# Performance work log

Hardware: AMD Instinct MI355X
Metric: run time of the kernel (lower is better)

Reference implementation:

```python
import jax, jax.numpy as jnp
import numpy as np

B, L, H, N = 8, 2048, 512, 64  # batch, seq_len, d_model, SSM state size


def setup_inputs() -> dict:
    key = jax.random.key(0)
    ks = jax.random.split(key, 10)
    x = jax.random.normal(ks[0], (B, L, H), jnp.float32)
    # S4D-style parameters (diagonal SSM, S4D-Lin init)
    log_dt = jnp.log(1e-3) + jax.random.uniform(ks[1], (H,), jnp.float32) * (jnp.log(1e-1) - jnp.log(1e-3))
    A_re = -0.5 * jnp.ones((H, N), jnp.float32)
    A_im = jnp.tile(np.pi * jnp.arange(N, dtype=np.float32), (H, 1))
    C_re = jax.random.normal(ks[2], (H, N), jnp.float32) * (0.5 ** 0.5)
    C_im = jax.random.normal(ks[3], (H, N), jnp.float32) * (0.5 ** 0.5)
    D_skip = jax.random.normal(ks[4], (H,), jnp.float32)
    # S4 output linear (GLU): d_model -> 2*d_model, then gated
    W_out = jax.random.normal(ks[5], (2 * H, H), jnp.float32) / np.sqrt(H)
    b_out = jnp.zeros((2 * H,), jnp.float32)
    # LayerNorms
    g1 = jnp.ones((H,), jnp.float32); beta1 = jnp.zeros((H,), jnp.float32)
    g2 = jnp.ones((H,), jnp.float32); beta2 = jnp.zeros((H,), jnp.float32)
    # 1x1 conv FFN (kernel_size=1 => pointwise linear), d_ff = d_model
    W1 = jax.random.normal(ks[6], (H, H), jnp.float32) / np.sqrt(H)
    bc1 = jnp.zeros((H,), jnp.float32)
    W2 = jax.random.normal(ks[7], (H, H), jnp.float32) / np.sqrt(H)
    bc2 = jnp.zeros((H,), jnp.float32)
    return dict(x=x, log_dt=log_dt, A_re=A_re, A_im=A_im, C_re=C_re, C_im=C_im,
                D_skip=D_skip, W_out=W_out, b_out=b_out, g1=g1, beta1=beta1,
                g2=g2, beta2=beta2, W1=W1, bc1=bc1, W2=W2, bc2=bc2)


def _layer_norm(x, g, b):
    mu = jnp.mean(x, axis=-1, keepdims=True)
    var = jnp.mean((x - mu) ** 2, axis=-1, keepdims=True)
    return (x - mu) / jnp.sqrt(var + 1e-5) * g + b


def _s4(x, log_dt, A_re, A_im, C_re, C_im, D_skip, W_out, b_out):
    # x: (B, L, H) channels-last (transposed=False)
    Lx = x.shape[1]
    dt = jnp.exp(log_dt)                       # (H,)
    A = A_re + 1j * A_im                       # (H, N) diagonal state matrix
    dtA = A * dt[:, None]
    # ZOH discretization of C: Ct = C * (exp(dt*A) - 1) / A
    Ct = (C_re + 1j * C_im) * ((jnp.exp(dtA) - 1.0) / A)
    # Vandermonde kernel: K[h, l] = 2 Re sum_n Ct[h,n] exp(dt*A[h,n]*l)
    l = jnp.arange(Lx, dtype=jnp.float32)
    K = 2.0 * jnp.real(jnp.einsum('hn,hnl->hl', Ct, jnp.exp(dtA[:, :, None] * l)))
    # FFT long convolution (linear conv via zero-padded circular conv)
    u = jnp.swapaxes(x, 1, 2)                  # (B, H, L)
    n = 2 * Lx
    y = jnp.fft.irfft(jnp.fft.rfft(u, n) * jnp.fft.rfft(K, n)[None], n)[..., :Lx]
    y = y + D_skip[None, :, None] * u          # skip connection D*u
    y = jax.nn.gelu(y)                         # S4 default activation
    # output linear + GLU (S4 default postact)
    z = jnp.einsum('bhl,fh->bfl', y, W_out) + b_out[None, :, None]
    a, g = jnp.split(z, 2, axis=1)
    y = a * jax.nn.sigmoid(g)
    return jnp.swapaxes(y, 1, 2)               # (B, L, H)


def reference(x, log_dt, A_re, A_im, C_re, C_im, D_skip, W_out, b_out,
              g1, beta1, g2, beta2, W1, bc1, W2, bc2):
    new_x = _s4(x, log_dt, A_re, A_im, C_re, C_im, D_skip, W_out, b_out)
    x = x + new_x
    x = _layer_norm(x, g1, beta1)
    # FFN via 1x1 convs (pointwise linears); dropout is identity in eval
    y = jax.nn.relu(jnp.einsum('blh,fh->blf', x, W1) + bc1)
    y = jnp.einsum('blf,hf->blh', y, W2) + bc2
    return _layer_norm(x + y, g2, beta2)
```

## Files before the change

### kernel.cpp

```cpp
#include <hip/hip_runtime.h>
#include <cstddef>
#include <cstdint>

#define B_DIM 8
#define L_DIM 2048
#define H_DIM 512
#define N_DIM 64
#define HN (H_DIM * N_DIM)
#define BLH (B_DIM * L_DIM * H_DIM)
#define M_DIM (B_DIM * L_DIM)

typedef unsigned short u16;
typedef short bf16x8 __attribute__((ext_vector_type(8)));
typedef float floatx4 __attribute__((ext_vector_type(4)));

__device__ __forceinline__ float sigmoidf_(float v) {
    return 1.0f / (1.0f + __expf(-v));
}

__device__ __forceinline__ float gelu_tanh_(float x) {
    float x3 = x * x * x;
    float z = 0.7978845608028654f * fmaf(0.044715f, x3, x);
    float e = __expf(-2.0f * fabsf(z));
    float th = (1.0f - e) / (1.0f + e);
    th = copysignf(th, z);
    return 0.5f * x * (1.0f + th);
}

__device__ __forceinline__ u16 f2b(float f) {
    unsigned u = __float_as_uint(f);
    unsigned r = (u + 0x7fffu + ((u >> 16) & 1u)) >> 16;
    return (u16)r;
}
__device__ __forceinline__ float b2f(u16 u) {
    return __uint_as_float(((unsigned)u) << 16);
}
__device__ __forceinline__ void unpack2(unsigned u, float& a, float& b) {
    a = __uint_as_float(u << 16);
    b = __uint_as_float(u & 0xffff0000u);
}
__device__ __forceinline__ unsigned pack2(float a, float b) {
    return (unsigned)f2b(a) | ((unsigned)f2b(b) << 16);
}

__device__ __forceinline__ void csq(float& r, float& i) {
    float nr = r * r - i * i;
    i = 2.0f * r * i;
    r = nr;
}

__global__ __launch_bounds__(256) void cast_kernel(
    const float* __restrict__ src, u16* __restrict__ dst)
{
    int i = blockIdx.x * 256 + threadIdx.x;
    float4 v = *(const float4*)(src + (size_t)i * 4);
    uint2 p;
    p.x = pack2(v.x, v.y);
    p.y = pack2(v.z, v.w);
    *(uint2*)(dst + (size_t)i * 4) = p;
}

__global__ __launch_bounds__(256) void precompute_kernel(
    const float* __restrict__ log_dt, const float* __restrict__ A_re,
    const float* __restrict__ A_im, const float* __restrict__ C_re,
    const float* __restrict__ C_im, float* __restrict__ P)
{
    int i = blockIdx.x * 256 + threadIdx.x;
    if (i >= HN) return;
    int h = i >> 6;
    float dt = expf(log_dt[h]);
    float Ar = A_re[i], Ai = A_im[i];
    float ar = dt * Ar, ai = dt * Ai;
    float e = expf(ar);
    float wr = e * cosf(ai);
    float wi = e * sinf(ai);
    float em1r = wr - 1.0f, em1i = wi;
    float inv = 1.0f / fmaf(Ar, Ar, Ai * Ai);
    float qr = fmaf(em1r, Ar, em1i * Ai) * inv;
    float qi = fmaf(em1i, Ar, -(em1r * Ai)) * inv;
    float Cr = C_re[i], Ci = C_im[i];
    float ctr = Cr * qr - Ci * qi;
    float cti = Cr * qi + Ci * qr;
    P[i]          = wr;
    P[HN + i]     = wi;
    P[2 * HN + i] = 2.0f * ctr;
    P[3 * HN + i] = 2.0f * cti;
}

__global__ __launch_bounds__(256) void ktab_kernel(
    const float* __restrict__ P, float* __restrict__ Ktab)
{
    int wv = threadIdx.x >> 6, lane = threadIdx.x & 63;
    int h = blockIdx.x * 4 + wv;
    int pidx = (h << 6) + lane;
    float wr = P[pidx], wi = P[HN + pidx];
    float c2r = P[2 * HN + pidx], c2i = P[3 * HN + pidx];
    float pr = 1.0f, pi = 0.0f;
    for (int tau = 0; tau < 64; ++tau) {
        float term = c2r * pr - c2i * pi;
        #pragma unroll
        for (int m = 32; m > 0; m >>= 1) term += __shfl_xor(term, m, 64);
        if (lane == 0) Ktab[(h << 6) + tau] = term;
        float nr = pr * wr - pi * wi, ni = pr * wi + pi * wr;
        pr = nr; pi = ni;
    }
}

__global__ __launch_bounds__(256) void toepfill_kernel(
    const float* __restrict__ Ktab, u16* __restrict__ Toep_bf)
{
    int idx = blockIdx.x * 256 + threadIdx.x;
    int h = idx >> 12;
    int rem = idx & 4095;
    int tt = rem >> 6, j = rem & 63;
    u16 v = 0;
    if (j <= tt) v = f2b(Ktab[(h << 6) + (tt - j)]);
    Toep_bf[idx] = v;
}

__global__ __launch_bounds__(256) void xtrans_kernel(
    const float* __restrict__ x, u16* __restrict__ XT)
{
    __shared__ float tile[32][33];
    int b  = blockIdx.z;
    int l0 = blockIdx.x * 32;
    int h0 = blockIdx.y * 32;
    int tx = threadIdx.x & 31;
    int ty = threadIdx.x >> 5;
    #pragma unroll
    for (int r = 0; r < 4; ++r)
        tile[ty + r * 8][tx] = x[((size_t)b * L_DIM + l0 + ty + r * 8) * H_DIM + h0 + tx];
    __syncthreads();
    #pragma unroll
    for (int r = 0; r < 4; ++r)
        XT[((size_t)b * H_DIM + h0 + ty + r * 8) * L_DIM + l0 + tx] = f2b(tile[tx][ty + r * 8]);
}

__global__ __launch_bounds__(256) void ssm_chunk_kernel(
    const u16* __restrict__ XT, const float* __restrict__ P,
    const u16* __restrict__ Toep_bf, const float* __restrict__ D_skip,
    u16* __restrict__ YT)
{
    __shared__ u16 U[128 * 72];
    __shared__ u16 S[128 * 136];
    __shared__ u16 EVT[13312];
    u16* E  = EVT;
    u16* Tp = EVT;
    u16* V  = EVT + 4608;

    const int h    = blockIdx.x;
    const int b0   = blockIdx.y * 4;
    const int t    = threadIdx.x;
    const int lane = t & 63;
    const int wv   = t >> 6;
    const int lm   = lane & 15, lq = lane >> 4;

    const int pidx = (h << 6) + lane;
    const float wr  = P[pidx],          wi  = P[HN + pidx];
    const float c2r = P[2 * HN + pidx], c2i = P[3 * HN + pidx];

    #pragma unroll
    for (int r = 0; r < 4; ++r) {
        int idx = t + r * 256;
        int row = idx >> 3, ch = idx & 7;
        const u16* gp = XT + (((size_t)(b0 + (row >> 5)) * H_DIM + h) << 11)
                           + ((row & 31) << 6) + (ch << 3);
        *(uint4*)&U[row * 72 + ch * 8] = *(const uint4*)gp;
    }

    float bwr, bwi;
    {
        float g16r = wr, g16i = wi;
        csq(g16r, g16i); csq(g16r, g16i); csq(g16r, g16i); csq(g16r, g16i);
        if (wv == 0)      { bwr = 1.0f; bwi = 0.0f; }
        else if (wv == 1) { bwr = g16r; bwi = g16i; }
        else if (wv == 2) { bwr = g16r; bwi = g16i; csq(bwr, bwi); }
        else {
            float g32r = g16r, g32i = g16i; csq(g32r, g32i);
            bwr = g32r * g16r - g32i * g16i;
            bwi = g32r * g16i + g32i * g16r;
        }
    }

    {
        float pr = bwr, pi = bwi;
        #pragma unroll
        for (int jk = 0; jk < 16; ++jk) {
            int k = (wv << 4) + jk;
            int j = 63 - k;
            E[(2 * lane) * 72 + j]     = f2b(pr);
            E[(2 * lane + 1) * 72 + j] = f2b(pi);
            float nr = pr * wr - pi * wi, ni = pr * wi + pi * wr;
            pr = nr; pi = ni;
        }
    }
    __syncthreads();

    {
        const int wm = wv >> 1, wn = wv & 1;
        floatx4 acc[4][4] = {};
        #pragma unroll
        for (int ks = 0; ks < 2; ++ks) {
            bf16x8 af[4], bfv[4];
            #pragma unroll
            for (int i = 0; i < 4; ++i)
                af[i] = *(const bf16x8*)&E[(wm * 64 + i * 16 + lm) * 72 + ks * 32 + lq * 8];
            #pragma unroll
            for (int j = 0; j < 4; ++j)
                bfv[j] = *(const bf16x8*)&U[(wn * 64 + j * 16 + lm) * 72 + ks * 32 + lq * 8];
            #pragma unroll
            for (int i = 0; i < 4; ++i) {
                #pragma unroll
                for (int j = 0; j < 4; ++j)
                    acc[i][j] = __builtin_amdgcn_mfma_f32_16x16x32_bf16(af[i], bfv[j], acc[i][j], 0, 0, 0);
            }
        }
        #pragma unroll
        for (int i = 0; i < 4; ++i) {
            #pragma unroll
            for (int j = 0; j < 4; ++j) {
                int ncol = wn * 64 + j * 16 + lm;
                int m0   = wm * 64 + i * 16 + lq * 4;
                u16 pk[4];
                #pragma unroll
                for (int r = 0; r < 4; ++r) pk[r] = f2b(acc[i][j][r]);
                *(uint2*)&S[ncol * 136 + m0] = *(uint2*)pk;
            }
        }
    }
    __syncthreads();

    {
        float pr = bwr, pi = bwi;
        {
            float nr = pr * wr - pi * wi, ni = pr * wi + pi * wr;
            pr = nr; pi = ni;
        }
        #pragma unroll
        for (int jk = 1; jk <= 16; ++jk) {
            int tr = (wv << 4) + jk - 1;
            float qr = c2r * pr - c2i * pi;
            float qi = c2r * pi + c2i * pr;
            V[tr * 136 + 2 * lane]     = f2b(qr);
            V[tr * 136 + 2 * lane + 1] = f2b(-qi);
            float nr = pr * wr - pi * wi, ni = pr * wi + pi * wr;
            pr = nr; pi = ni;
        }
        #pragma unroll
        for (int r = 0; r < 2; ++r) {
            int idx = t + r * 256;
            int row = idx >> 3, ch = idx & 7;
            *(uint4*)&Tp[row * 72 + ch * 8] =
                *(const uint4*)&Toep_bf[((size_t)h << 12) + (row << 6) + (ch << 3)];
        }
        float wTr = wr, wTi = wi;
        csq(wTr, wTi); csq(wTr, wTi); csq(wTr, wTi);
        csq(wTr, wTi); csq(wTr, wTi); csq(wTr, wTi);
        float Sr = 0.0f, Si = 0.0f;
        const int n2 = lane * 2;
        for (int c = 0; c < 32; ++c) {
            int base = (wv * 32 + c) * 136 + n2;
            unsigned lv = *(unsigned*)&S[base];
            float lr, li;
            unpack2(lv, lr, li);
            *(unsigned*)&S[base] = pack2(Sr, Si);
            float nSr = wTr * Sr - wTi * Si + lr;
            Si = wTr * Si + wTi * Sr + li;
            Sr = nSr;
        }
    }
    __syncthreads();

    {
        const float Dh = D_skip[h];
        floatx4 acc[4][2] = {};
        #pragma unroll
        for (int ks = 0; ks < 6; ++ks) {
            bf16x8 af[4], bfv[2];
            if (ks < 2) {
                #pragma unroll
                for (int i = 0; i < 4; ++i)
                    af[i] = *(const bf16x8*)&Tp[(i * 16 + lm) * 72 + ks * 32 + lq * 8];
                #pragma unroll
                for (int j = 0; j < 2; ++j)
                    bfv[j] = *(const bf16x8*)&U[(wv * 32 + j * 16 + lm) * 72 + ks * 32 + lq * 8];
            } else {
                #pragma unroll
                for (int i = 0; i < 4; ++i)
                    af[i] = *(const bf16x8*)&V[(i * 16 + lm) * 136 + (ks - 2) * 32 + lq * 8];
                #pragma unroll
                for (int j = 0; j < 2; ++j)
                    bfv[j] = *(const bf16x8*)&S[(wv * 32 + j * 16 + lm) * 136 + (ks - 2) * 32 + lq * 8];
            }
            #pragma unroll
            for (int i = 0; i < 4; ++i) {
                #pragma unroll
                for (int j = 0; j < 2; ++j)
                    acc[i][j] = __builtin_amdgcn_mfma_f32_16x16x32_bf16(af[i], bfv[j], acc[i][j], 0, 0, 0);
            }
        }
        #pragma unroll
        for (int j = 0; j < 2; ++j) {
            int ncol = wv * 32 + j * 16 + lm;
            int bloc = ncol >> 5, c = ncol & 31;
            size_t gbase = (((size_t)(b0 + bloc) * H_DIM + h) << 11) + (c << 6);
            #pragma unroll
            for (int i = 0; i < 4; ++i) {
                int t0 = i * 16 + lq * 4;
                u16 upk[4];
                *(uint2*)upk = *(const uint2*)&U[ncol * 72 + t0];
                u16 opk[4];
                #pragma unroll
                for (int r = 0; r < 4; ++r) {
                    float uvv = b2f(upk[r]);
                    float yv = gelu_tanh_(fmaf(Dh, uvv, acc[i][j][r]));
                    opk[r] = f2b(yv);
                }
                *(uint2*)&YT[gbase + t0] = *(uint2*)opk;
            }
        }
    }
}

__global__ __launch_bounds__(256) void ytrans_kernel(
    const u16* __restrict__ YT, u16* __restrict__ Y)
{
    __shared__ u16 tile[32][33];
    int b  = blockIdx.z;
    int l0 = blockIdx.x * 32;
    int h0 = blockIdx.y * 32;
    int tx = threadIdx.x & 31;
    int ty = threadIdx.x >> 5;
    #pragma unroll
    for (int r = 0; r < 4; ++r)
        tile[ty + r * 8][tx] = YT[((size_t)b * H_DIM + h0 + ty + r * 8) * L_DIM + l0 + tx];
    __syncthreads();
    #pragma unroll
    for (int r = 0; r < 4; ++r)
        Y[((size_t)b * L_DIM + l0 + ty + r * 8) * H_DIM + h0 + tx] = tile[tx][ty + r * 8];
}

__device__ __forceinline__ void stage_tile_512(
    const u16* __restrict__ g, u16* lds, int row0, int k0)
{
    const int t = threadIdx.x;
    const int row  = t >> 2;
    const int csrc = (t & 3) ^ ((t >> 3) & 3);
    const u16* gp = g + (size_t)(row0 + row) * 512 + k0 + csrc * 8;
    __builtin_amdgcn_global_load_lds(
        (const __attribute__((address_space(1))) unsigned int*)gp,
        (__attribute__((address_space(3))) unsigned int*)(lds + (size_t)t * 8),
        16, 0, 0);
}

__global__ __launch_bounds__(512) void gemm1_glu_kernel(
    const u16* __restrict__ A, const u16* __restrict__ Wo,
    const float* __restrict__ bo, const float* __restrict__ x,
    u16* __restrict__ out)
{
    __shared__ u16 As[2][128 * 32];
    __shared__ u16 Ba[2][128 * 32];
    __shared__ u16 Bg[2][128 * 32];
    const int t    = threadIdx.x;
    const int lane = t & 63;
    const int wv   = t >> 6;
    const int wm   = wv >> 2, wn = wv & 3;
    const int lm   = lane & 15, lq = lane >> 4;
    const int sw   = (lq ^ ((lm >> 1) & 3)) * 8;
    const int m0   = blockIdx.x * 128, n0 = blockIdx.y * 128;
    floatx4 accA[4][2] = {};
    floatx4 accG[4][2] = {};

    stage_tile_512(A, As[0], m0, 0);
    stage_tile_512(Wo, Ba[0], n0, 0);
    stage_tile_512(Wo, Bg[0], 512 + n0, 0);
    __syncthreads();

    int cur = 0;
    for (int k0 = 32; k0 < 512; k0 += 32) {
        const int nx = cur ^ 1;
        stage_tile_512(A, As[nx], m0, k0);
        stage_tile_512(Wo, Ba[nx], n0, k0);
        stage_tile_512(Wo, Bg[nx], 512 + n0, k0);

        bf16x8 af[4], ba[2], bg[2];
        #pragma unroll
        for (int i = 0; i < 4; ++i)
            af[i] = *(const bf16x8*)&As[cur][(wm * 64 + i * 16 + lm) * 32 + sw];
        #pragma unroll
        for (int j = 0; j < 2; ++j) {
            ba[j] = *(const bf16x8*)&Ba[cur][(wn * 32 + j * 16 + lm) * 32 + sw];
            bg[j] = *(const bf16x8*)&Bg[cur][(wn * 32 + j * 16 + lm) * 32 + sw];
        }
        #pragma unroll
        for (int i = 0; i < 4; ++i) {
            #pragma unroll
            for (int j = 0; j < 2; ++j) {
                accA[i][j] = __builtin_amdgcn_mfma_f32_16x16x32_bf16(af[i], ba[j], accA[i][j], 0, 0, 0);
                accG[i][j] = __builtin_amdgcn_mfma_f32_16x16x32_bf16(af[i], bg[j], accG[i][j], 0, 0, 0);
            }
        }
        __syncthreads();
        cur = nx;
    }
    {
        bf16x8 af[4], ba[2], bg[2];
        #pragma unroll
        for (int i = 0; i < 4; ++i)
            af[i] = *(const bf16x8*)&As[cur][(wm * 64 + i * 16 + lm) * 32 + sw];
        #pragma unroll
        for (int j = 0; j < 2; ++j) {
            ba[j] = *(const bf16x8*)&Ba[cur][(wn * 32 + j * 16 + lm) * 32 + sw];
            bg[j] = *(const bf16x8*)&Bg[cur][(wn * 32 + j * 16 + lm) * 32 + sw];
        }
        #pragma unroll
        for (int i = 0; i < 4; ++i) {
            #pragma unroll
            for (int j = 0; j < 2; ++j) {
                accA[i][j] = __builtin_amdgcn_mfma_f32_16x16x32_bf16(af[i], ba[j], accA[i][j], 0, 0, 0);
                accG[i][j] = __builtin_amdgcn_mfma_f32_16x16x32_bf16(af[i], bg[j], accG[i][j], 0, 0, 0);
            }
        }
    }
    #pragma unroll
    for (int j = 0; j < 2; ++j) {
        int n = n0 + wn * 32 + j * 16 + lm;
        float bav = bo[n], bgv = bo[512 + n];
        #pragma unroll
        for (int i = 0; i < 4; ++i) {
            #pragma unroll
            for (int r = 0; r < 4; ++r) {
                int m = m0 + wm * 64 + i * 16 + lq * 4 + r;
                float av = accA[i][j][r] + bav;
                float gv = accG[i][j][r] + bgv;
                float xv = x[(size_t)m * 512 + n];
                out[(size_t)m * 512 + n] = f2b(fmaf(av, sigmoidf_(gv), xv));
            }
        }
    }
}

template<int EPI>
__global__ __launch_bounds__(512) void gemm_bt_bf_kernel(
    const u16* __restrict__ A, const u16* __restrict__ Bw,
    const float* __restrict__ bias, u16* __restrict__ C)
{
    __shared__ u16 As[2][128 * 32];
    __shared__ u16 Bs[2][128 * 32];
    const int t    = threadIdx.x;
    const int lane = t & 63;
    const int wv   = t >> 6;
    const int wm   = wv >> 2, wn = wv & 3;
    const int lm   = lane & 15, lq = lane >> 4;
    const int sw   = (lq ^ ((lm >> 1) & 3)) * 8;
    const int m0   = blockIdx.x * 128, n0 = blockIdx.y * 128;
    floatx4 acc[4][2] = {};

    stage_tile_512(A, As[0], m0, 0);
    stage_tile_512(Bw, Bs[0], n0, 0);
    __syncthreads();

    int cur = 0;
    for (int k0 = 32; k0 < 512; k0 += 32) {
        const int nx = cur ^ 1;
        stage_tile_512(A, As[nx], m0, k0);
        stage_tile_512(Bw, Bs[nx], n0, k0);

        bf16x8 af[4], bfr[2];
        #pragma unroll
        for (int i = 0; i < 4; ++i)
            af[i] = *(const bf16x8*)&As[cur][(wm * 64 + i * 16 + lm) * 32 + sw];
        #pragma unroll
        for (int j = 0; j < 2; ++j)
            bfr[j] = *(const bf16x8*)&Bs[cur][(wn * 32 + j * 16 + lm) * 32 + sw];
        #pragma unroll
        for (int i = 0; i < 4; ++i) {
            #pragma unroll
            for (int j = 0; j < 2; ++j)
                acc[i][j] = __builtin_amdgcn_mfma_f32_16x16x32_bf16(af[i], bfr[j], acc[i][j], 0, 0, 0);
        }
        __syncthreads();
        cur = nx;
    }
    {
        bf16x8 af[4], bfr[2];
        #pragma unroll
        for (int i = 0; i < 4; ++i)
            af[i] = *(const bf16x8*)&As[cur][(wm * 64 + i * 16 + lm) * 32 + sw];
        #pragma unroll
        for (int j = 0; j < 2; ++j)
            bfr[j] = *(const bf16x8*)&Bs[cur][(wn * 32 + j * 16 + lm) * 32 + sw];
        #pragma unroll
        for (int i = 0; i < 4; ++i) {
            #pragma unroll
            for (int j = 0; j < 2; ++j)
                acc[i][j] = __builtin_amdgcn_mfma_f32_16x16x32_bf16(af[i], bfr[j], acc[i][j], 0, 0, 0);
        }
    }
    #pragma unroll
    for (int j = 0; j < 2; ++j) {
        int n = n0 + wn * 32 + j * 16 + lm;
        float bv = bias[n];
        #pragma unroll
        for (int i = 0; i < 4; ++i) {
            #pragma unroll
            for (int r = 0; r < 4; ++r) {
                int m = m0 + wm * 64 + i * 16 + lq * 4 + r;
                float v = acc[i][j][r] + bv;
                if (EPI == 1) v = fmaxf(v, 0.0f);
                C[(size_t)m * 512 + n] = f2b(v);
            }
        }
    }
}

template<bool HASRES, bool F32OUT>
__global__ __launch_bounds__(256) void ln_bf_kernel(
    const u16* __restrict__ in, const u16* __restrict__ res,
    const float* __restrict__ gamma, const float* __restrict__ beta,
    u16* __restrict__ outb, float* __restrict__ outf)
{
    int w    = threadIdx.x >> 6;
    int lane = threadIdx.x & 63;
    size_t row  = (size_t)blockIdx.x * 4 + w;
    size_t base = row * 512 + lane * 8;
    uint4 raw = *(const uint4*)(in + base);
    float v[8];
    unpack2(raw.x, v[0], v[1]); unpack2(raw.y, v[2], v[3]);
    unpack2(raw.z, v[4], v[5]); unpack2(raw.w, v[6], v[7]);
    if (HASRES) {
        uint4 rr = *(const uint4*)(res + base);
        float rv[8];
        unpack2(rr.x, rv[0], rv[1]); unpack2(rr.y, rv[2], rv[3]);
        unpack2(rr.z, rv[4], rv[5]); unpack2(rr.w, rv[6], rv[7]);
        #pragma unroll
        for (int i = 0; i < 8; ++i) v[i] += rv[i];
    }
    float s = 0.0f, sq = 0.0f;
    #pragma unroll
    for (int i = 0; i < 8; ++i) { s += v[i]; sq = fmaf(v[i], v[i], sq); }
    #pragma unroll
    for (int m = 32; m > 0; m >>= 1) {
        s  += __shfl_xor(s, m, 64);
        sq += __shfl_xor(sq, m, 64);
    }
    float mu  = s * (1.0f / 512.0f);
    float var = sq * (1.0f / 512.0f) - mu * mu;
    float rs  = rsqrtf(var + 1e-5f);
    float g[8], bt[8];
    *(float4*)&g[0]  = *(const float4*)(gamma + lane * 8);
    *(float4*)&g[4]  = *(const float4*)(gamma + lane * 8 + 4);
    *(float4*)&bt[0] = *(const float4*)(beta + lane * 8);
    *(float4*)&bt[4] = *(const float4*)(beta + lane * 8 + 4);
    float o[8];
    #pragma unroll
    for (int i = 0; i < 8; ++i)
        o[i] = fmaf((v[i] - mu) * rs, g[i], bt[i]);
    if (F32OUT) {
        *(float4*)(outf + base)     = *(float4*)&o[0];
        *(float4*)(outf + base + 4) = *(float4*)&o[4];
    } else {
        uint4 p;
        p.x = pack2(o[0], o[1]); p.y = pack2(o[2], o[3]);
        p.z = pack2(o[4], o[5]); p.w = pack2(o[6], o[7]);
        *(uint4*)(outb + base) = p;
    }
}

extern "C" void kernel_launch(void* const* d_in, const int* in_sizes, int n_in,
                              void* d_out, int out_size, void* d_ws, size_t ws_size,
                              hipStream_t stream)
{
    (void)in_sizes; (void)n_in; (void)out_size; (void)ws_size;
    const float* x      = (const float*)d_in[0];
    const float* log_dt = (const float*)d_in[1];
    const float* A_re   = (const float*)d_in[2];
    const float* A_im   = (const float*)d_in[3];
    const float* C_re   = (const float*)d_in[4];
    const float* C_im   = (const float*)d_in[5];
    const float* D_skip = (const float*)d_in[6];
    const float* W_out  = (const float*)d_in[7];
    const float* b_out  = (const float*)d_in[8];
    const float* g1     = (const float*)d_in[9];
    const float* beta1  = (const float*)d_in[10];
    const float* g2     = (const float*)d_in[11];
    const float* beta2  = (const float*)d_in[12];
    const float* W1     = (const float*)d_in[13];
    const float* bc1    = (const float*)d_in[14];
    const float* W2     = (const float*)d_in[15];
    const float* bc2    = (const float*)d_in[16];
    float* out = (float*)d_out;

    char*  wsb    = (char*)d_ws;
    float* P      = (float*)wsb;
    float* Ktab   = (float*)(wsb + 4 * HN * 4);
    u16*   Toep   = (u16*)(wsb + 4 * HN * 4 + 512 * 64 * 4);
    u16*   Wobf   = Toep + 512 * 4096;
    u16*   W1bf   = Wobf + 1024 * 512;
    u16*   W2bf   = W1bf + 512 * 512;
    u16*   r1     = W2bf + 512 * 512;
    u16*   r2     = r1 + BLH;
    u16*   r3     = r2 + BLH;

    cast_kernel<<<512, 256, 0, stream>>>(W_out, Wobf);
    cast_kernel<<<256, 256, 0, stream>>>(W1, W1bf);
    cast_kernel<<<256, 256, 0, stream>>>(W2, W2bf);
    precompute_kernel<<<HN / 256, 256, 0, stream>>>(log_dt, A_re, A_im, C_re, C_im, P);
    ktab_kernel<<<128, 256, 0, stream>>>(P, Ktab);
    toepfill_kernel<<<8192, 256, 0, stream>>>(Ktab, Toep);
    xtrans_kernel<<<dim3(L_DIM / 32, H_DIM / 32, B_DIM), 256, 0, stream>>>(x, r1);
    ssm_chunk_kernel<<<dim3(H_DIM, 2), 256, 0, stream>>>(r1, P, Toep, D_skip, r2);
    ytrans_kernel<<<dim3(L_DIM / 32, H_DIM / 32, B_DIM), 256, 0, stream>>>(r2, r3);
    gemm1_glu_kernel<<<dim3(M_DIM / 128, 4), 512, 0, stream>>>(r3, Wobf, b_out, x, r2);
    ln_bf_kernel<false, false><<<M_DIM / 4, 256, 0, stream>>>(r2, nullptr, g1, beta1, r1, nullptr);
    gemm_bt_bf_kernel<1><<<dim3(M_DIM / 128, 4), 512, 0, stream>>>(r1, W1bf, bc1, r3);
    gemm_bt_bf_kernel<0><<<dim3(M_DIM / 128, 4), 512, 0, stream>>>(r3, W2bf, bc2, r2);
    ln_bf_kernel<true, true><<<M_DIM / 4, 256, 0, stream>>>(r2, r1, g2, beta2, nullptr, out);
}
```

Baseline: 250.6 us.

## Fuse second FFN GEMM with residual LayerNorm and merge small setup kernels

```diff
diff --git a/kernel.cpp b/kernel.cpp
--- a/kernel.cpp
+++ b/kernel.cpp
@@ -49,10 +49,17 @@
     r = nr;
 }
 
-__global__ __launch_bounds__(256) void cast_kernel(
-    const float* __restrict__ src, u16* __restrict__ dst)
-{
-    int i = blockIdx.x * 256 + threadIdx.x;
+__global__ __launch_bounds__(256) void cast3_kernel(
+    const float* __restrict__ s0, const float* __restrict__ s1,
+    const float* __restrict__ s2, u16* __restrict__ d0,
+    u16* __restrict__ d1, u16* __restrict__ d2)
+{
+    int bid = blockIdx.x;
+    const float* src; u16* dst; int off;
+    if (bid < 512)      { src = s0; dst = d0; off = bid; }
+    else if (bid < 768) { src = s1; dst = d1; off = bid - 512; }
+    else                { src = s2; dst = d2; off = bid - 768; }
+    int i = off * 256 + threadIdx.x;
     float4 v = *(const float4*)(src + (size_t)i * 4);
     uint2 p;
     p.x = pack2(v.x, v.y);
@@ -60,14 +67,18 @@
     *(uint2*)(dst + (size_t)i * 4) = p;
 }
 
-__global__ __launch_bounds__(256) void precompute_kernel(
+__global__ __launch_bounds__(256) void params_kernel(
     const float* __restrict__ log_dt, const float* __restrict__ A_re,
     const float* __restrict__ A_im, const float* __restrict__ C_re,
-    const float* __restrict__ C_im, float* __restrict__ P)
-{
-    int i = blockIdx.x * 256 + threadIdx.x;
-    if (i >= HN) return;
-    int h = i >> 6;
+    const float* __restrict__ C_im, float* __restrict__ P,
+    u16* __restrict__ Toep_bf)
+{
+    __shared__ float ktab_s[4][64];
+    const int t = threadIdx.x;
+    const int wv = t >> 6, lane = t & 63;
+    const int i = blockIdx.x * 256 + t;
+    const int h = i >> 6;
+
     float dt = expf(log_dt[h]);
     float Ar = A_re[i], Ai = A_im[i];
     float ar = dt * Ar, ai = dt * Ai;
@@ -79,43 +90,38 @@
     float qr = fmaf(em1r, Ar, em1i * Ai) * inv;
     float qi = fmaf(em1i, Ar, -(em1r * Ai)) * inv;
     float Cr = C_re[i], Ci = C_im[i];
-    float ctr = Cr * qr - Ci * qi;
-    float cti = Cr * qi + Ci * qr;
+    float c2r = 2.0f * (Cr * qr - Ci * qi);
+    float c2i = 2.0f * (Cr * qi + Ci * qr);
     P[i]          = wr;
     P[HN + i]     = wi;
-    P[2 * HN + i] = 2.0f * ctr;
-    P[3 * HN + i] = 2.0f * cti;
-}
-
-__global__ __launch_bounds__(256) void ktab_kernel(
-    const float* __restrict__ P, float* __restrict__ Ktab)
-{
-    int wv = threadIdx.x >> 6, lane = threadIdx.x & 63;
-    int h = blockIdx.x * 4 + wv;
-    int pidx = (h << 6) + lane;
-    float wr = P[pidx], wi = P[HN + pidx];
-    float c2r = P[2 * HN + pidx], c2i = P[3 * HN + pidx];
+    P[2 * HN + i] = c2r;
+    P[3 * HN + i] = c2i;
+
     float pr = 1.0f, pi = 0.0f;
     for (int tau = 0; tau < 64; ++tau) {
         float term = c2r * pr - c2i * pi;
         #pragma unroll
         for (int m = 32; m > 0; m >>= 1) term += __shfl_xor(term, m, 64);
-        if (lane == 0) Ktab[(h << 6) + tau] = term;
+        if (lane == 0) ktab_s[wv][tau] = term;
         float nr = pr * wr - pi * wi, ni = pr * wi + pi * wr;
         pr = nr; pi = ni;
     }
-}
-
-__global__ __launch_bounds__(256) void toepfill_kernel(
-    const float* __restrict__ Ktab, u16* __restrict__ Toep_bf)
-{
-    int idx = blockIdx.x * 256 + threadIdx.x;
-    int h = idx >> 12;
-    int rem = idx & 4095;
-    int tt = rem >> 6, j = rem & 63;
-    u16 v = 0;
-    if (j <= tt) v = f2b(Ktab[(h << 6) + (tt - j)]);
-    Toep_bf[idx] = v;
+    __syncthreads();
+
+    const int h0 = blockIdx.x * 4;
+    #pragma unroll
+    for (int r = 0; r < 8; ++r) {
+        int c = t + r * 256;
+        int hh = c >> 9, rem = c & 511;
+        int tt = rem >> 3, j0 = (rem & 7) * 8;
+        u16 vv[8];
+        #pragma unroll
+        for (int jj = 0; jj < 8; ++jj) {
+            int j = j0 + jj;
+            vv[jj] = (j <= tt) ? f2b(ktab_s[hh][tt - j]) : (u16)0;
+        }
+        *(uint4*)&Toep_bf[((size_t)(h0 + hh) << 12) + (tt << 6) + j0] = *(uint4*)vv;
+    }
 }
 
 __global__ __launch_bounds__(256) void xtrans_kernel(
@@ -440,8 +446,7 @@
     }
 }
 
-template<int EPI>
-__global__ __launch_bounds__(512) void gemm_bt_bf_kernel(
+__global__ __launch_bounds__(512) void gemm_relu_kernel(
     const u16* __restrict__ A, const u16* __restrict__ Bw,
     const float* __restrict__ bias, u16* __restrict__ C)
 {
@@ -506,19 +511,172 @@
             #pragma unroll
             for (int r = 0; r < 4; ++r) {
                 int m = m0 + wm * 64 + i * 16 + lq * 4 + r;
-                float v = acc[i][j][r] + bv;
-                if (EPI == 1) v = fmaxf(v, 0.0f);
+                float v = fmaxf(acc[i][j][r] + bv, 0.0f);
                 C[(size_t)m * 512 + n] = f2b(v);
             }
         }
     }
 }
 
-template<bool HASRES, bool F32OUT>
+__global__ __launch_bounds__(512) void gemm2_ln_kernel(
+    const u16* __restrict__ A, const u16* __restrict__ Bw,
+    const float* __restrict__ bias, const u16* __restrict__ res,
+    const float* __restrict__ gamma, const float* __restrict__ beta,
+    float* __restrict__ out)
+{
+    __shared__ u16 As[2][32 * 32];
+    __shared__ u16 Bs[2][512 * 32];
+    __shared__ float2 lnred[32 * 8];
+    const int t    = threadIdx.x;
+    const int lane = t & 63;
+    const int wv   = t >> 6;
+    const int lm   = lane & 15, lq = lane >> 4;
+    const int sw   = (lq ^ ((lm >> 1) & 3)) * 8;
+    const int m0   = blockIdx.x * 32;
+    floatx4 acc[2][4] = {};
+
+    const int csrc = (t & 3) ^ ((t >> 3) & 3);
+
+    {
+        #pragma unroll
+        for (int r = 0; r < 4; ++r) {
+            int row = (t >> 2) + r * 128;
+            const u16* gp = Bw + (size_t)row * 512 + csrc * 8;
+            __builtin_amdgcn_global_load_lds(
+                (const __attribute__((address_space(1))) unsigned int*)gp,
+                (__attribute__((address_space(3))) unsigned int*)(&Bs[0][0] + (size_t)t * 8 + (size_t)r * 4096),
+                16, 0, 0);
+        }
+        if (t < 128) {
+            int row = t >> 2;
+            const u16* gp = A + (size_t)(m0 + row) * 512 + csrc * 8;
+            __builtin_amdgcn_global_load_lds(
+                (const __attribute__((address_space(1))) unsigned int*)gp,
+                (__attribute__((address_space(3))) unsigned int*)(&As[0][0] + (size_t)t * 8),
+                16, 0, 0);
+        }
+    }
+    __syncthreads();
+
+    int cur = 0;
+    for (int k0 = 32; k0 < 512; k0 += 32) {
+        const int nx = cur ^ 1;
+        #pragma unroll
+        for (int r = 0; r < 4; ++r) {
+            int row = (t >> 2) + r * 128;
+            const u16* gp = Bw + (size_t)row * 512 + k0 + csrc * 8;
+            __builtin_amdgcn_global_load_lds(
+                (const __attribute__((address_space(1))) unsigned int*)gp,
+                (__attribute__((address_space(3))) unsigned int*)(&Bs[nx][0] + (size_t)t * 8 + (size_t)r * 4096),
+                16, 0, 0);
+        }
+        if (t < 128) {
+            int row = t >> 2;
+            const u16* gp = A + (size_t)(m0 + row) * 512 + k0 + csrc * 8;
+            __builtin_amdgcn_global_load_lds(
+                (const __attribute__((address_space(1))) unsigned int*)gp,
+                (__attribute__((address_space(3))) unsigned int*)(&As[nx][0] + (size_t)t * 8),
+                16, 0, 0);
+        }
+
+        bf16x8 af[2], bfr[4];
+        #pragma unroll
+        for (int i = 0; i < 2; ++i)
+            af[i] = *(const bf16x8*)&As[cur][(i * 16 + lm) * 32 + sw];
+        #pragma unroll
+        for (int j = 0; j < 4; ++j)
+            bfr[j] = *(const bf16x8*)&Bs[cur][(wv * 64 + j * 16 + lm) * 32 + sw];
+        #pragma unroll
+        for (int i = 0; i < 2; ++i) {
+            #pragma unroll
+            for (int j = 0; j < 4; ++j)
+                acc[i][j] = __builtin_amdgcn_mfma_f32_16x16x32_bf16(af[i], bfr[j], acc[i][j], 0, 0, 0);
+        }
+        __syncthreads();
+        cur = nx;
+    }
+    {
+        bf16x8 af[2], bfr[4];
+        #pragma unroll
+        for (int i = 0; i < 2; ++i)
+            af[i] = *(const bf16x8*)&As[cur][(i * 16 + lm) * 32 + sw];
+        #pragma unroll
+        for (int j = 0; j < 4; ++j)
+            bfr[j] = *(const bf16x8*)&Bs[cur][(wv * 64 + j * 16 + lm) * 32 + sw];
+        #pragma unroll
+        for (int i = 0; i < 2; ++i) {
+            #pragma unroll
+            for (int j = 0; j < 4; ++j)
+                acc[i][j] = __builtin_amdgcn_mfma_f32_16x16x32_bf16(af[i], bfr[j], acc[i][j], 0, 0, 0);
+        }
+    }
+
+    float bv[4], gv[4], btv[4];
+    #pragma unroll
+    for (int j = 0; j < 4; ++j) {
+        int n = wv * 64 + j * 16 + lm;
+        bv[j]  = bias[n];
+        gv[j]  = gamma[n];
+        btv[j] = beta[n];
+    }
+    #pragma unroll
+    for (int i = 0; i < 2; ++i) {
+        #pragma unroll
+        for (int j = 0; j < 4; ++j) {
+            int n = wv * 64 + j * 16 + lm;
+            #pragma unroll
+            for (int r = 0; r < 4; ++r) {
+                int m = m0 + i * 16 + lq * 4 + r;
+                acc[i][j][r] += bv[j] + b2f(res[(size_t)m * 512 + n]);
+            }
+        }
+    }
+    #pragma unroll
+    for (int i = 0; i < 2; ++i) {
+        #pragma unroll
+        for (int r = 0; r < 4; ++r) {
+            float s  = acc[i][0][r] + acc[i][1][r] + acc[i][2][r] + acc[i][3][r];
+            float sq = acc[i][0][r] * acc[i][0][r] + acc[i][1][r] * acc[i][1][r]
+                     + acc[i][2][r] * acc[i][2][r] + acc[i][3][r] * acc[i][3][r];
+            #pragma unroll
+            for (int msk = 1; msk < 16; msk <<= 1) {
+                s  += __shfl_xor(s, msk, 64);
+                sq += __shfl_xor(sq, msk, 64);
+            }
+            if (lm == 0) {
+                float2 p; p.x = s; p.y = sq;
+                lnred[(i * 16 + lq * 4 + r) * 8 + wv] = p;
+            }
+        }
+    }
+    __syncthreads();
+    #pragma unroll
+    for (int i = 0; i < 2; ++i) {
+        #pragma unroll
+        for (int r = 0; r < 4; ++r) {
+            int row = i * 16 + lq * 4 + r;
+            float s = 0.0f, sq = 0.0f;
+            #pragma unroll
+            for (int w = 0; w < 8; ++w) {
+                float2 p = lnred[row * 8 + w];
+                s += p.x; sq += p.y;
+            }
+            float mu  = s * (1.0f / 512.0f);
+            float var = sq * (1.0f / 512.0f) - mu * mu;
+            float rs  = rsqrtf(var + 1e-5f);
+            #pragma unroll
+            for (int j = 0; j < 4; ++j) {
+                int n = wv * 64 + j * 16 + lm;
+                out[(size_t)(m0 + row) * 512 + n] = fmaf((acc[i][j][r] - mu) * rs, gv[j], btv[j]);
+            }
+        }
+    }
+}
+
 __global__ __launch_bounds__(256) void ln_bf_kernel(
-    const u16* __restrict__ in, const u16* __restrict__ res,
+    const u16* __restrict__ in,
     const float* __restrict__ gamma, const float* __restrict__ beta,
-    u16* __restrict__ outb, float* __restrict__ outf)
+    u16* __restrict__ outb)
 {
     int w    = threadIdx.x >> 6;
     int lane = threadIdx.x & 63;
@@ -528,14 +686,6 @@
     float v[8];
     unpack2(raw.x, v[0], v[1]); unpack2(raw.y, v[2], v[3]);
     unpack2(raw.z, v[4], v[5]); unpack2(raw.w, v[6], v[7]);
-    if (HASRES) {
-        uint4 rr = *(const uint4*)(res + base);
-        float rv[8];
-        unpack2(rr.x, rv[0], rv[1]); unpack2(rr.y, rv[2], rv[3]);
-        unpack2(rr.z, rv[4], rv[5]); unpack2(rr.w, rv[6], rv[7]);
-        #pragma unroll
-        for (int i = 0; i < 8; ++i) v[i] += rv[i];
-    }
     float s = 0.0f, sq = 0.0f;
     #pragma unroll
     for (int i = 0; i < 8; ++i) { s += v[i]; sq = fmaf(v[i], v[i], sq); }
@@ -556,15 +706,10 @@
     #pragma unroll
     for (int i = 0; i < 8; ++i)
         o[i] = fmaf((v[i] - mu) * rs, g[i], bt[i]);
-    if (F32OUT) {
-        *(float4*)(outf + base)     = *(float4*)&o[0];
-        *(float4*)(outf + base + 4) = *(float4*)&o[4];
-    } else {
-        uint4 p;
-        p.x = pack2(o[0], o[1]); p.y = pack2(o[2], o[3]);
-        p.z = pack2(o[4], o[5]); p.w = pack2(o[6], o[7]);
-        *(uint4*)(outb + base) = p;
-    }
+    uint4 p;
+    p.x = pack2(o[0], o[1]); p.y = pack2(o[2], o[3]);
+    p.z = pack2(o[4], o[5]); p.w = pack2(o[6], o[7]);
+    *(uint4*)(outb + base) = p;
 }
 
 extern "C" void kernel_launch(void* const* d_in, const int* in_sizes, int n_in,
@@ -593,7 +738,6 @@
 
     char*  wsb    = (char*)d_ws;
     float* P      = (float*)wsb;
-    float* Ktab   = (float*)(wsb + 4 * HN * 4);
     u16*   Toep   = (u16*)(wsb + 4 * HN * 4 + 512 * 64 * 4);
     u16*   Wobf   = Toep + 512 * 4096;
     u16*   W1bf   = Wobf + 1024 * 512;
@@ -602,18 +746,13 @@
     u16*   r2     = r1 + BLH;
     u16*   r3     = r2 + BLH;
 
-    cast_kernel<<<512, 256, 0, stream>>>(W_out, Wobf);
-    cast_kernel<<<256, 256, 0, stream>>>(W1, W1bf);
-    cast_kernel<<<256, 256, 0, stream>>>(W2, W2bf);
-    precompute_kernel<<<HN / 256, 256, 0, stream>>>(log_dt, A_re, A_im, C_re, C_im, P);
-    ktab_kernel<<<128, 256, 0, stream>>>(P, Ktab);
-    toepfill_kernel<<<8192, 256, 0, stream>>>(Ktab, Toep);
+    cast3_kernel<<<1024, 256, 0, stream>>>(W_out, W1, W2, Wobf, W1bf, W2bf);
+    params_kernel<<<128, 256, 0, stream>>>(log_dt, A_re, A_im, C_re, C_im, P, Toep);
     xtrans_kernel<<<dim3(L_DIM / 32, H_DIM / 32, B_DIM), 256, 0, stream>>>(x, r1);
     ssm_chunk_kernel<<<dim3(H_DIM, 2), 256, 0, stream>>>(r1, P, Toep, D_skip, r2);
     ytrans_kernel<<<dim3(L_DIM / 32, H_DIM / 32, B_DIM), 256, 0, stream>>>(r2, r3);
     gemm1_glu_kernel<<<dim3(M_DIM / 128, 4), 512, 0, stream>>>(r3, Wobf, b_out, x, r2);
-    ln_bf_kernel<false, false><<<M_DIM / 4, 256, 0, stream>>>(r2, nullptr, g1, beta1, r1, nullptr);
-    gemm_bt_bf_kernel<1><<<dim3(M_DIM / 128, 4), 512, 0, stream>>>(r1, W1bf, bc1, r3);
-    gemm_bt_bf_kernel<0><<<dim3(M_DIM / 128, 4), 512, 0, stream>>>(r3, W2bf, bc2, r2);
-    ln_bf_kernel<true, true><<<M_DIM / 4, 256, 0, stream>>>(r2, r1, g2, beta2, nullptr, out);
-}
+    ln_bf_kernel<<<M_DIM / 4, 256, 0, stream>>>(r2, g1, beta1, r1);
+    gemm_relu_kernel<<<dim3(M_DIM / 128, 4), 512, 0, stream>>>(r1, W1bf, bc1, r3);
+    gemm2_ln_kernel<<<M_DIM / 32, 512, 0, stream>>>(r3, W2bf, bc2, r1, g2, beta2, out);
+}
```

Result: faster. 245.1 us (-2.2%).
